# Optimization experiments

Measured on AMD Instinct MI355X. Metric: run time of the kernel, lower is better.

## Reference

```python
import jax, jax.numpy as jnp
import numpy as np

DIM = 1024
N_SLOTS = 8
RANK = 256
T = 1024
B = 8
SPECTRAL_RADIUS = 0.99


def setup_inputs() -> dict:
    key = jax.random.key(0)
    ks = jax.random.split(key, 6)
    x = jax.random.normal(ks[0], (T, B, DIM), dtype=jnp.float32)
    z = jax.random.normal(ks[1], (T, B, DIM), dtype=jnp.float32)
    h0 = jnp.zeros((B, N_SLOTS, DIM), dtype=jnp.float32)
    # parameters (xavier-ish / scaled as in _init_weights)
    W_x = jax.random.normal(ks[2], (DIM, DIM), dtype=jnp.float32) * (1.0 / np.sqrt(DIM))
    U = jax.random.normal(ks[3], (N_SLOTS, DIM, RANK), dtype=jnp.float32) * (SPECTRAL_RADIUS * 0.3 / np.sqrt(DIM))
    V = jax.random.normal(ks[4], (N_SLOTS, RANK, DIM), dtype=jnp.float32) * (0.5 / np.sqrt(DIM))
    b = jnp.zeros((DIM,), dtype=jnp.float32)
    C = jnp.ones((N_SLOTS,), dtype=jnp.float32) / N_SLOTS
    return {"x": x, "z": z, "h0": h0, "W_x": W_x, "U": U, "V": V, "b": b, "C": C}


def reference(x, z, h0, W_x, U, V, b, C):
    # x, z: [T, B, D]; h0: [B, S, D]
    def step(h_prev, xz):
        x_t, z_t = xz                               # [B, D] each
        Wx = x_t @ W_x.T                            # [B, D]
        Vh = jnp.einsum('bsd,srd->bsr', h_prev, V)  # [B, S, R]
        Uh = jnp.einsum('bsr,sdr->bsd', Vh, U)      # [B, S, D]
        h_new = jnp.tanh(Wx[:, None, :] + Uh + b)   # [B, S, D]
        h_comb = jnp.einsum('bsd,s->bd', h_new, C)  # [B, D]
        out = h_comb * jax.nn.silu(z_t)             # [B, D]
        return h_new, (h_new, out)

    _, (hs, output) = jax.lax.scan(step, h0, (x, z))
    # hs: [T, B, S, D]; prepend h0 -> [T+1, B, S, D] -> permute to [T+1, S, B, D]
    h = jnp.concatenate([h0[None], hs], axis=0)
    h = jnp.transpose(h, (0, 2, 1, 3))
    return output, h
```

## Files before the change

kernel.cpp:

```cpp
#include <hip/hip_runtime.h>
#include <cstdint>
#include <cstddef>

#define DIM 1024
#define NS 8
#define RANK 256
#define TSTEPS 1024
#define BB 8
#define NG 8
#define DCH 128

typedef __attribute__((ext_vector_type(8))) short s8v;
typedef __attribute__((ext_vector_type(4))) short s4v;
typedef __attribute__((ext_vector_type(4))) float f4v;
typedef __attribute__((ext_vector_type(2))) float f2v;

__device__ __forceinline__ unsigned short f2bf(float f) {
  unsigned u = __float_as_uint(f);
  u += 0x7fffu + ((u >> 16) & 1u);
  return (unsigned short)(u >> 16);
}
__device__ __forceinline__ float bf2f(unsigned short h) {
  return __uint_as_float(((unsigned)h) << 16);
}

__global__ void init_kernel(const float* __restrict__ h0, float* __restrict__ hOut0,
                            unsigned int* __restrict__ cnt) {
  int i = blockIdx.x * blockDim.x + threadIdx.x;
  const int NH = NS * BB * DIM;
  if (i < NH) {
    int s = i >> 13, b = (i >> 10) & 7, d = i & 1023;
    hOut0[i] = h0[((size_t)b * NS + s) * DIM + d];
  }
  if (i < 128) cnt[i] = 0u;
}

__global__ __launch_bounds__(256) void gemm_wx(const float* __restrict__ X,
                                               const float* __restrict__ W,
                                               float* __restrict__ Co) {
  __shared__ unsigned short As[128][40];
  __shared__ unsigned short Bh[128][40];
  __shared__ unsigned short Bl[128][40];
  const int bn = blockIdx.x & 7;
  const int bm = blockIdx.x >> 3;
  const int tid = threadIdx.x;
  const int wave = tid >> 6, lane = tid & 63, l15 = lane & 15, quad = lane >> 4;
  const int wm = wave & 1, wn = wave >> 1;
  f4v acc[4][4];
  for (int i = 0; i < 4; ++i)
    for (int j = 0; j < 4; ++j) acc[i][j] = (f4v){0.f, 0.f, 0.f, 0.f};
  const int row = tid >> 1, kh = (tid & 1) * 16;
  const float* srcA = X + ((size_t)(bm * 128 + row)) * DIM + kh;
  const float* srcB = W + ((size_t)(bn * 128 + row)) * DIM + kh;
  for (int k0 = 0; k0 < DIM; k0 += 32) {
    __syncthreads();
    unsigned short ta[16], th[16], tl[16];
    for (int q = 0; q < 16; q += 4) {
      f4v a4 = *(const f4v*)(srcA + k0 + q);
      for (int r2 = 0; r2 < 4; ++r2) ta[q + r2] = f2bf(a4[r2]);
      f4v b4 = *(const f4v*)(srcB + k0 + q);
      for (int r2 = 0; r2 < 4; ++r2) {
        unsigned short hi = f2bf(b4[r2]);
        th[q + r2] = hi;
        tl[q + r2] = f2bf(b4[r2] - bf2f(hi));
      }
    }
    *(s8v*)&As[row][kh] = *(s8v*)&ta[0];
    *(s8v*)&As[row][kh + 8] = *(s8v*)&ta[8];
    *(s8v*)&Bh[row][kh] = *(s8v*)&th[0];
    *(s8v*)&Bh[row][kh + 8] = *(s8v*)&th[8];
    *(s8v*)&Bl[row][kh] = *(s8v*)&tl[0];
    *(s8v*)&Bl[row][kh + 8] = *(s8v*)&tl[8];
    __syncthreads();
    s8v af[4], bhf[4], blf[4];
    for (int i = 0; i < 4; ++i) af[i] = *(const s8v*)&As[wm * 64 + i * 16 + l15][quad * 8];
    for (int j = 0; j < 4; ++j) bhf[j] = *(const s8v*)&Bh[wn * 64 + j * 16 + l15][quad * 8];
    for (int j = 0; j < 4; ++j) blf[j] = *(const s8v*)&Bl[wn * 64 + j * 16 + l15][quad * 8];
    for (int i = 0; i < 4; ++i)
      for (int j = 0; j < 4; ++j) {
        acc[i][j] = __builtin_amdgcn_mfma_f32_16x16x32_bf16(af[i], bhf[j], acc[i][j], 0, 0, 0);
        acc[i][j] = __builtin_amdgcn_mfma_f32_16x16x32_bf16(af[i], blf[j], acc[i][j], 0, 0, 0);
      }
  }
  for (int i = 0; i < 4; ++i)
    for (int j = 0; j < 4; ++j) {
      int ci = bm * 128 + wm * 64 + i * 16 + quad * 4;
      int cd = bn * 128 + wn * 64 + j * 16 + l15;
      for (int r2 = 0; r2 < 4; ++r2)
        Co[((size_t)(ci + r2)) * DIM + cd] = acc[i][j][r2];
    }
}

__global__ __launch_bounds__(256) void seq_kernel(const float* __restrict__ Wx,
                                                  float* __restrict__ hOut,
                                                  const float* __restrict__ bias,
                                                  const float* __restrict__ U,
                                                  const float* __restrict__ V,
                                                  const float* __restrict__ h0,
                                                  float* __restrict__ vx,
                                                  unsigned int* __restrict__ cnt) {
  const int s = blockIdx.x & 7;
  const int g = blockIdx.x >> 3;
  const int tid = threadIdx.x;
  const int wave = tid >> 6, lane = tid & 63, l15 = lane & 15, quad = lane >> 4;
  const int d0 = g * DCH;

  __shared__ unsigned short hbuf[16][DCH + 8];
  __shared__ unsigned short vbuf[16][RANK + 8];

  s8v Vfrag[4][4];
  #pragma unroll
  for (int mt = 0; mt < 4; ++mt)
    #pragma unroll
    for (int kk = 0; kk < 4; ++kk) {
      const float* p = V + ((size_t)s * RANK + wave * 64 + mt * 16 + l15) * DIM
                         + d0 + kk * 32 + quad * 8;
      s8v f;
      #pragma unroll
      for (int j = 0; j < 8; ++j) f[j] = (short)f2bf(p[j]);
      Vfrag[mt][kk] = f;
    }
  s8v Ufrag[2][8];
  #pragma unroll
  for (int mt = 0; mt < 2; ++mt)
    #pragma unroll
    for (int kk = 0; kk < 8; ++kk) {
      const float* p = U + ((size_t)s * DIM + d0 + wave * 32 + mt * 16 + l15) * RANK
                         + kk * 32 + quad * 8;
      s8v f;
      #pragma unroll
      for (int j = 0; j < 8; ++j) f[j] = (short)f2bf(p[j]);
      Ufrag[mt][kk] = f;
    }
  float bias4[2][4];
  #pragma unroll
  for (int mt = 0; mt < 2; ++mt)
    #pragma unroll
    for (int r2 = 0; r2 < 4; ++r2)
      bias4[mt][r2] = bias[d0 + wave * 32 + mt * 16 + quad * 4 + r2];

  for (int c = tid; c < BB * DCH; c += 256) {
    int b = c >> 7, dl = c & 127;
    hbuf[b][dl] = f2bf(h0[((size_t)b * NS + s) * DIM + d0 + dl]);
  }
  __syncthreads();

  unsigned int* cA = cnt + s * 16;
  const int b_ep = l15;

  for (int t = 0; t < TSTEPS; ++t) {
    const int buf = t & 1;
    f4v acc1[4];
    #pragma unroll
    for (int mt = 0; mt < 4; ++mt) acc1[mt] = (f4v){0.f, 0.f, 0.f, 0.f};
    #pragma unroll
    for (int kk = 0; kk < 4; ++kk) {
      s8v hfrag = *(const s8v*)&hbuf[l15][kk * 32 + quad * 8];
      #pragma unroll
      for (int mt = 0; mt < 4; ++mt)
        acc1[mt] = __builtin_amdgcn_mfma_f32_16x16x32_bf16(Vfrag[mt][kk], hfrag, acc1[mt], 0, 0, 0);
    }
    f4v wx4[2];
    if (b_ep < 8) {
      #pragma unroll
      for (int mt = 0; mt < 2; ++mt)
        wx4[mt] = *(const f4v*)&Wx[((size_t)t * BB + b_ep) * DIM + d0 + wave * 32 + mt * 16 + quad * 4];
    }
    {
      unsigned long long* vw = (unsigned long long*)vx
          + ((size_t)(s * 2 + buf) * NG + g) * 1024 + (size_t)l15 * 128;
      if (l15 < 8) {
        #pragma unroll
        for (int mt = 0; mt < 4; ++mt) {
          int half = wave * 32 + mt * 8 + quad * 2;
          union { f2v f; unsigned long long u; } c0, c1;
          c0.f = (f2v){acc1[mt][0], acc1[mt][1]};
          c1.f = (f2v){acc1[mt][2], acc1[mt][3]};
          __hip_atomic_store(vw + half, c0.u, __ATOMIC_RELAXED, __HIP_MEMORY_SCOPE_AGENT);
          __hip_atomic_store(vw + half + 1, c1.u, __ATOMIC_RELAXED, __HIP_MEMORY_SCOPE_AGENT);
        }
      }
    }
    asm volatile("s_waitcnt vmcnt(0)" ::: "memory");
    __syncthreads();
    if (tid == 0) {
      __hip_atomic_fetch_add(cA, 1u, __ATOMIC_RELAXED, __HIP_MEMORY_SCOPE_AGENT);
      const unsigned tgt = (unsigned)(NG * (t + 1));
      while (__hip_atomic_load(cA, __ATOMIC_RELAXED, __HIP_MEMORY_SCOPE_AGENT) < tgt) {}
    }
    __syncthreads();
    {
      const int b = tid >> 5, r0 = (tid & 31) * 8;
      const unsigned long long* vr = (const unsigned long long*)vx
          + ((size_t)(s * 2 + buf) * NG) * 1024 + (size_t)b * 128 + (tid & 31) * 4;
      float sum[8] = {0.f, 0.f, 0.f, 0.f, 0.f, 0.f, 0.f, 0.f};
      #pragma unroll
      for (int g2 = 0; g2 < NG; ++g2) {
        #pragma unroll
        for (int q = 0; q < 4; ++q) {
          unsigned long long u = __hip_atomic_load(vr + (size_t)g2 * 1024 + q,
                                                   __ATOMIC_RELAXED, __HIP_MEMORY_SCOPE_AGENT);
          union { unsigned long long u; f2v f; } c; c.u = u;
          sum[q * 2] += c.f[0];
          sum[q * 2 + 1] += c.f[1];
        }
      }
      s8v v8;
      #pragma unroll
      for (int j = 0; j < 8; ++j) v8[j] = (short)f2bf(sum[j]);
      *(s8v*)&vbuf[b][r0] = v8;
    }
    __syncthreads();
    f4v acc2[2];
    acc2[0] = (f4v){0.f, 0.f, 0.f, 0.f};
    acc2[1] = (f4v){0.f, 0.f, 0.f, 0.f};
    #pragma unroll
    for (int kk = 0; kk < 8; ++kk) {
      s8v vfrag = *(const s8v*)&vbuf[l15][kk * 32 + quad * 8];
      acc2[0] = __builtin_amdgcn_mfma_f32_16x16x32_bf16(Ufrag[0][kk], vfrag, acc2[0], 0, 0, 0);
      acc2[1] = __builtin_amdgcn_mfma_f32_16x16x32_bf16(Ufrag[1][kk], vfrag, acc2[1], 0, 0, 0);
    }
    if (b_ep < 8) {
      #pragma unroll
      for (int mt = 0; mt < 2; ++mt) {
        int dl = wave * 32 + mt * 16 + quad * 4;
        f4v h4;
        s4v hb;
        #pragma unroll
        for (int r2 = 0; r2 < 4; ++r2) {
          float u = acc2[mt][r2] + wx4[mt][r2] + bias4[mt][r2];
          u = fminf(fmaxf(u, -15.f), 15.f);
          float e = __expf(2.f * u);
          float hv = (e - 1.f) / (e + 1.f);
          h4[r2] = hv;
          hb[r2] = (short)f2bf(hv);
        }
        *(f4v*)&hOut[(((size_t)(t + 1) * NS + s) * BB + b_ep) * DIM + d0 + dl] = h4;
        *(s4v*)&hbuf[b_ep][dl] = hb;
      }
    }
    __syncthreads();
  }
}

__global__ void out_kernel(const float* __restrict__ z, const float* __restrict__ h,
                           const float* __restrict__ Cs, float* __restrict__ out) {
  size_t i = (size_t)blockIdx.x * blockDim.x + threadIdx.x;
  const size_t n4 = (size_t)TSTEPS * BB * DIM / 4;
  float c[8];
  for (int s2 = 0; s2 < 8; ++s2) c[s2] = Cs[s2];
  for (; i < n4; i += (size_t)gridDim.x * blockDim.x) {
    size_t base = i * 4;
    size_t t = base / (BB * DIM);
    size_t rem = base % (BB * DIM);
    f4v accv = (f4v){0.f, 0.f, 0.f, 0.f};
    for (int s2 = 0; s2 < 8; ++s2) {
      f4v hv = *(const f4v*)&h[((t + 1) * NS + s2) * (size_t)(BB * DIM) + rem];
      accv += hv * c[s2];
    }
    f4v zv = *(const f4v*)&z[base];
    f4v o;
    for (int r2 = 0; r2 < 4; ++r2) {
      float zz = zv[r2];
      float sil = zz / (1.f + __expf(-zz));
      o[r2] = accv[r2] * sil;
    }
    *(f4v*)&out[base] = o;
  }
}

extern "C" void kernel_launch(void* const* d_in, const int* in_sizes, int n_in,
                              void* d_out, int out_size, void* d_ws, size_t ws_size,
                              hipStream_t stream) {
  const float* x  = (const float*)d_in[0];
  const float* z  = (const float*)d_in[1];
  const float* h0 = (const float*)d_in[2];
  const float* Wm = (const float*)d_in[3];
  const float* U  = (const float*)d_in[4];
  const float* V  = (const float*)d_in[5];
  const float* bs = (const float*)d_in[6];
  const float* Cs = (const float*)d_in[7];

  float* out  = (float*)d_out;
  float* hOut = out + (size_t)TSTEPS * BB * DIM;

  float* vx = (float*)d_ws;
  unsigned int* cnt = (unsigned int*)(vx + (size_t)NS * 2 * NG * BB * RANK);

  float* Wx = out;

  init_kernel<<<256, 256, 0, stream>>>(h0, hOut, cnt);
  gemm_wx<<<512, 256, 0, stream>>>(x, Wm, Wx);
  seq_kernel<<<64, 256, 0, stream>>>(Wx, hOut, bs, U, V, h0, vx, cnt);
  out_kernel<<<2048, 256, 0, stream>>>(z, hOut, Cs, out);
}
```

Measured before the change: 4.848 ms.

## Replace atomic counter barrier with per-block step tags polled by all threads

```diff
diff --git a/kernel.cpp b/kernel.cpp
--- a/kernel.cpp
+++ b/kernel.cpp
@@ -25,14 +25,14 @@
 }
 
 __global__ void init_kernel(const float* __restrict__ h0, float* __restrict__ hOut0,
-                            unsigned int* __restrict__ cnt) {
+                            unsigned int* __restrict__ tags) {
   int i = blockIdx.x * blockDim.x + threadIdx.x;
   const int NH = NS * BB * DIM;
   if (i < NH) {
     int s = i >> 13, b = (i >> 10) & 7, d = i & 1023;
     hOut0[i] = h0[((size_t)b * NS + s) * DIM + d];
   }
-  if (i < 128) cnt[i] = 0u;
+  if (i < 128) tags[i] = 0u;
 }
 
 __global__ __launch_bounds__(256) void gemm_wx(const float* __restrict__ X,
@@ -98,7 +98,7 @@
                                                   const float* __restrict__ V,
                                                   const float* __restrict__ h0,
                                                   float* __restrict__ vx,
-                                                  unsigned int* __restrict__ cnt) {
+                                                  unsigned int* __restrict__ tags) {
   const int s = blockIdx.x & 7;
   const int g = blockIdx.x >> 3;
   const int tid = threadIdx.x;
@@ -145,11 +145,21 @@
   }
   __syncthreads();
 
-  unsigned int* cA = cnt + s * 16;
   const int b_ep = l15;
+  const int bpoll = tid >> 5;
+  const int rbase = (tid & 31) * 8;
 
   for (int t = 0; t < TSTEPS; ++t) {
     const int buf = t & 1;
+    const unsigned want = (unsigned)(t + 1);
+
+    f4v wx4[2];
+    if (b_ep < 8) {
+      #pragma unroll
+      for (int mt = 0; mt < 2; ++mt)
+        wx4[mt] = *(const f4v*)&Wx[((size_t)t * BB + b_ep) * DIM + d0 + wave * 32 + mt * 16 + quad * 4];
+    }
+
     f4v acc1[4];
     #pragma unroll
     for (int mt = 0; mt < 4; ++mt) acc1[mt] = (f4v){0.f, 0.f, 0.f, 0.f};
@@ -160,39 +170,41 @@
       for (int mt = 0; mt < 4; ++mt)
         acc1[mt] = __builtin_amdgcn_mfma_f32_16x16x32_bf16(Vfrag[mt][kk], hfrag, acc1[mt], 0, 0, 0);
     }
-    f4v wx4[2];
+
     if (b_ep < 8) {
-      #pragma unroll
-      for (int mt = 0; mt < 2; ++mt)
-        wx4[mt] = *(const f4v*)&Wx[((size_t)t * BB + b_ep) * DIM + d0 + wave * 32 + mt * 16 + quad * 4];
-    }
+      unsigned long long* vw = (unsigned long long*)vx
+          + ((size_t)(s * 2 + buf) * NG + g) * 1024 + (size_t)b_ep * 128;
+      #pragma unroll
+      for (int mt = 0; mt < 4; ++mt) {
+        int half = wave * 32 + mt * 8 + quad * 2;
+        union { f2v f; unsigned long long u; } c0, c1;
+        c0.f = (f2v){acc1[mt][0], acc1[mt][1]};
+        c1.f = (f2v){acc1[mt][2], acc1[mt][3]};
+        __hip_atomic_store(vw + half, c0.u, __ATOMIC_RELAXED, __HIP_MEMORY_SCOPE_AGENT);
+        __hip_atomic_store(vw + half + 1, c1.u, __ATOMIC_RELAXED, __HIP_MEMORY_SCOPE_AGENT);
+      }
+    }
+    asm volatile("s_waitcnt vmcnt(0)" ::: "memory");
+    __syncthreads();
+    if (tid == 0)
+      __hip_atomic_store(tags + (s * 2 + buf) * NG + g, want,
+                         __ATOMIC_RELAXED, __HIP_MEMORY_SCOPE_AGENT);
+
     {
-      unsigned long long* vw = (unsigned long long*)vx
-          + ((size_t)(s * 2 + buf) * NG + g) * 1024 + (size_t)l15 * 128;
-      if (l15 < 8) {
+      const unsigned int* tg = tags + (s * 2 + buf) * NG;
+      for (;;) {
+        unsigned bad = 0;
         #pragma unroll
-        for (int mt = 0; mt < 4; ++mt) {
-          int half = wave * 32 + mt * 8 + quad * 2;
-          union { f2v f; unsigned long long u; } c0, c1;
-          c0.f = (f2v){acc1[mt][0], acc1[mt][1]};
-          c1.f = (f2v){acc1[mt][2], acc1[mt][3]};
-          __hip_atomic_store(vw + half, c0.u, __ATOMIC_RELAXED, __HIP_MEMORY_SCOPE_AGENT);
-          __hip_atomic_store(vw + half + 1, c1.u, __ATOMIC_RELAXED, __HIP_MEMORY_SCOPE_AGENT);
-        }
-      }
-    }
-    asm volatile("s_waitcnt vmcnt(0)" ::: "memory");
-    __syncthreads();
-    if (tid == 0) {
-      __hip_atomic_fetch_add(cA, 1u, __ATOMIC_RELAXED, __HIP_MEMORY_SCOPE_AGENT);
-      const unsigned tgt = (unsigned)(NG * (t + 1));
-      while (__hip_atomic_load(cA, __ATOMIC_RELAXED, __HIP_MEMORY_SCOPE_AGENT) < tgt) {}
-    }
-    __syncthreads();
+        for (int g2 = 0; g2 < NG; ++g2)
+          bad |= __hip_atomic_load(tg + g2, __ATOMIC_RELAXED, __HIP_MEMORY_SCOPE_AGENT) ^ want;
+        if (!bad) break;
+      }
+    }
+    asm volatile("" ::: "memory");
+
     {
-      const int b = tid >> 5, r0 = (tid & 31) * 8;
       const unsigned long long* vr = (const unsigned long long*)vx
-          + ((size_t)(s * 2 + buf) * NG) * 1024 + (size_t)b * 128 + (tid & 31) * 4;
+          + ((size_t)(s * 2 + buf) * NG) * 1024 + (size_t)bpoll * 128 + (tid & 31) * 4;
       float sum[8] = {0.f, 0.f, 0.f, 0.f, 0.f, 0.f, 0.f, 0.f};
       #pragma unroll
       for (int g2 = 0; g2 < NG; ++g2) {
@@ -208,9 +220,10 @@
       s8v v8;
       #pragma unroll
       for (int j = 0; j < 8; ++j) v8[j] = (short)f2bf(sum[j]);
-      *(s8v*)&vbuf[b][r0] = v8;
-    }
-    __syncthreads();
+      *(s8v*)&vbuf[bpoll][rbase] = v8;
+    }
+    __syncthreads();
+
     f4v acc2[2];
     acc2[0] = (f4v){0.f, 0.f, 0.f, 0.f};
     acc2[1] = (f4v){0.f, 0.f, 0.f, 0.f};
@@ -285,12 +298,12 @@
   float* hOut = out + (size_t)TSTEPS * BB * DIM;
 
   float* vx = (float*)d_ws;
-  unsigned int* cnt = (unsigned int*)(vx + (size_t)NS * 2 * NG * BB * RANK);
+  unsigned int* tags = (unsigned int*)(vx + (size_t)NS * 2 * NG * BB * RANK);
 
   float* Wx = out;
 
-  init_kernel<<<256, 256, 0, stream>>>(h0, hOut, cnt);
+  init_kernel<<<256, 256, 0, stream>>>(h0, hOut, tags);
   gemm_wx<<<512, 256, 0, stream>>>(x, Wm, Wx);
-  seq_kernel<<<64, 256, 0, stream>>>(Wx, hOut, bs, U, V, h0, vx, cnt);
+  seq_kernel<<<64, 256, 0, stream>>>(Wx, hOut, bs, U, V, h0, vx, tags);
   out_kernel<<<2048, 256, 0, stream>>>(z, hOut, Cs, out);
 }
```

Result: no change. 4.873 ms (+0.5%).
